# Kernel optimization log

Hardware: AMD Instinct MI355X
Metric: run time of the kernel (lower is better)

Reference implementation:

```python
import jax, jax.numpy as jnp
import numpy as np

N = 50000      # nodes
E = 800000     # edges
IN_DIM = 16
D = 128        # latent_dim == d_model == num_heads*d_head
H = 8
DH = 16
DFF = 512
L = 3          # n_layers
CLAMP = 5.0
EPS = 1e-5


def _layer_norm(x, g, b):
    mu = jnp.mean(x, axis=-1, keepdims=True)
    var = jnp.mean((x - mu) ** 2, axis=-1, keepdims=True)
    return (x - mu) * jax.lax.rsqrt(var + EPS) * g + b


def setup_inputs() -> dict:
    key = jax.random.key(0)
    ks = jax.random.split(key, 16)
    def w(k, shape, fan_in):
        return jax.random.normal(k, shape, dtype=jnp.float32) * (1.0 / np.sqrt(fan_in))
    inp = {
        "nf": jax.random.normal(ks[0], (N, IN_DIM), dtype=jnp.float32),
        "src": jax.random.randint(ks[1], (E,), 0, N, dtype=jnp.int32),
        "dst": jax.random.randint(ks[2], (E,), 0, N, dtype=jnp.int32),
        "enc_W": w(ks[3], (D, IN_DIM), IN_DIM),
        "enc_b": jnp.zeros((D,), jnp.float32),
        "Wq": w(ks[4], (L, H * DH, D), D),
        "Wk": w(ks[5], (L, H * DH, D), D),
        "Wv": w(ks[6], (L, H * DH, D), D),
        "Wo": w(ks[7], (L, D, H * DH), H * DH),
        "ln1_g": jnp.ones((L, D), jnp.float32),
        "ln1_b": jnp.zeros((L, D), jnp.float32),
        "ffn_W1": w(ks[8], (L, DFF, D), D),
        "ffn_b1": jnp.zeros((L, DFF), jnp.float32),
        "ffn_W2": w(ks[9], (L, D, DFF), DFF),
        "ffn_b2": jnp.zeros((L, D), jnp.float32),
        "ln2_g": jnp.ones((L, D), jnp.float32),
        "ln2_b": jnp.zeros((L, D), jnp.float32),
        "dec_W": w(ks[10], (1, D), D),
        "dec_b": jnp.zeros((1,), jnp.float32),
    }
    return inp


def reference(nf, src, dst, enc_W, enc_b, Wq, Wk, Wv, Wo, ln1_g, ln1_b,
              ffn_W1, ffn_b1, ffn_W2, ffn_b2, ln2_g, ln2_b, dec_W, dec_b):
    h = nf @ enc_W.T + enc_b                       # [N, D]
    scale = 1.0 / np.sqrt(DH)
    for l in range(L):
        q = h @ Wq[l].T                            # [N, H*DH]
        k = h @ Wk[l].T
        v = h @ Wv[l].T
        qe = q[dst].reshape(E, H, DH)              # per-edge gather (dst query)
        ke = k[src].reshape(E, H, DH)
        u = jnp.sum(qe * ke, axis=-1) * scale      # [E, H]
        u = jnp.clip(u, -CLAMP, CLAMP)
        # edge_softmax: normalize over edges sharing the same dst node
        m = jax.ops.segment_max(u, dst, num_segments=N)   # [N, H]
        e = jnp.exp(u - m[dst])
        s = jax.ops.segment_sum(e, dst, num_segments=N)   # [N, H]
        a = e / s[dst]                             # [E, H]
        av = a[..., None] * v[src].reshape(E, H, DH)      # [E, H, DH]
        sum_av = jax.ops.segment_sum(av.reshape(E, H * DH), dst, num_segments=N)
        uh = sum_av @ Wo[l].T                      # [N, D]
        h1 = _layer_norm(h + uh, ln1_g[l], ln1_b[l])
        f = jax.nn.relu(h1 @ ffn_W1[l].T + ffn_b1[l]) @ ffn_W2[l].T + ffn_b2[l]
        h = _layer_norm(h1 + f, ln2_g[l], ln2_b[l])
    pred = h @ dec_W.T + dec_b                     # [N, 1]
    # BasicReadout('mean') over the single batched graph -> [1, 1]
    return jnp.mean(pred, axis=0, keepdims=True)
```

## Files before the change

### kernel.cpp

```cpp
#include <hip/hip_runtime.h>
#include <math.h>

static constexpr int D   = 128;
static constexpr int DFF = 512;
static constexpr int LAYERS = 3;
static constexpr float CLAMP_V = 5.0f;
static constexpr float LN_EPS = 1e-5f;

typedef unsigned short u16;
typedef unsigned int   u32;
typedef short bf16x8 __attribute__((ext_vector_type(8)));
typedef float f32x4  __attribute__((ext_vector_type(4)));

__device__ inline float4 ld4(const float* p){ return *reinterpret_cast<const float4*>(p); }
__device__ inline u16 f2bf(float f){ u32 u = __float_as_uint(f); return (u16)((u + 0x7fff + ((u>>16)&1)) >> 16); }
__device__ inline float bl(u32 u){ return __uint_as_float(u << 16); }
__device__ inline float bh(u32 u){ return __uint_as_float(u & 0xffff0000u); }

__device__ inline void gload_lds16(const void* g, void* l) {
  __builtin_amdgcn_global_load_lds(
      (const __attribute__((address_space(1))) void*)g,
      (__attribute__((address_space(3))) void*)l, 16, 0, 0);
}

__global__ __launch_bounds__(256) void count_kernel(const int* __restrict__ dst,
                                                    int* __restrict__ deg, int E)
{
  int e = blockIdx.x*256 + threadIdx.x;
  if (e < E) atomicAdd(&deg[dst[e]], 1);
}

__global__ __launch_bounds__(256) void scan_bsum(const int* __restrict__ deg,
                                                 int* __restrict__ bsum, int N)
{
  const int i0 = blockIdx.x*1024 + threadIdx.x*4;
  int s = 0;
  if (i0 + 3 < N) { int4 v = *(const int4*)&deg[i0]; s = v.x+v.y+v.z+v.w; }
  else { for (int t = 0; t < 4; t++) if (i0+t < N) s += deg[i0+t]; }
  #pragma unroll
  for (int off = 1; off < 64; off <<= 1) s += __shfl_xor(s, off);
  __shared__ int ws_[4];
  if ((threadIdx.x & 63) == 0) ws_[threadIdx.x >> 6] = s;
  __syncthreads();
  if (threadIdx.x == 0) bsum[blockIdx.x] = ws_[0]+ws_[1]+ws_[2]+ws_[3];
}

__global__ __launch_bounds__(64) void scan_bbase(int* __restrict__ bsum, int NB)
{
  const int tid = threadIdx.x;
  int base = 0;
  for (int c = 0; c < NB; c += 64) {
    const int idx = c + tid;
    int v = (idx < NB) ? bsum[idx] : 0;
    const int orig = v;
    #pragma unroll
    for (int off = 1; off < 64; off <<= 1) {
      int t = __shfl_up(v, off);
      if (tid >= off) v += t;
    }
    if (idx < NB) bsum[idx] = base + v - orig;
    base += __shfl(v, 63);
  }
}

__global__ __launch_bounds__(256) void scan_write(const int* __restrict__ deg,
    const int* __restrict__ bbase, int* __restrict__ offs, int* __restrict__ cursor, int N)
{
  const int i0 = blockIdx.x*1024 + threadIdx.x*4;
  int v[4] = {0,0,0,0};
  if (i0 + 3 < N) { int4 t = *(const int4*)&deg[i0]; v[0]=t.x; v[1]=t.y; v[2]=t.z; v[3]=t.w; }
  else { for (int t = 0; t < 4; t++) if (i0+t < N) v[t] = deg[i0+t]; }
  const int s = v[0]+v[1]+v[2]+v[3];
  const int lane = threadIdx.x & 63, w = threadIdx.x >> 6;
  int inc = s;
  #pragma unroll
  for (int off = 1; off < 64; off <<= 1) {
    int t = __shfl_up(inc, off);
    if (lane >= off) inc += t;
  }
  __shared__ int wsum[4];
  if (lane == 63) wsum[w] = inc;
  __syncthreads();
  int wb = 0;
  for (int t = 0; t < 4; t++) if (t < w) wb += wsum[t];
  int run = bbase[blockIdx.x] + wb + inc - s;
  #pragma unroll
  for (int t = 0; t < 4; t++) {
    if (i0 + t < N) { offs[i0+t] = run; cursor[i0+t] = run; run += v[t]; }
  }
  if (i0 <= N-1 && N-1 < i0+4) offs[N] = run;
}

__global__ __launch_bounds__(256) void fill_kernel(const int* __restrict__ dst,
    const int* __restrict__ src, int* __restrict__ cursor, int* __restrict__ csr_src, int E)
{
  int e = blockIdx.x*256 + threadIdx.x;
  if (e < E) {
    int p = atomicAdd(&cursor[dst[e]], 1);
    csr_src[p] = src[e];
  }
}

__global__ __launch_bounds__(256) void convert_weights(
    const float* __restrict__ Wq, const float* __restrict__ Wk, const float* __restrict__ Wv,
    const float* __restrict__ Wo, const float* __restrict__ W1, const float* __restrict__ W2,
    u16* __restrict__ out)
{
  const int SQKV = 3*384*128;
  const int SWO  = 3*128*128;
  const int SW1  = 3*512*128;
  const int SW2  = 3*128*512;
  int i = blockIdx.x*256 + threadIdx.x;
  if (i >= SQKV+SWO+SW1+SW2) return;
  float v;
  if (i < SQKV) {
    int l = i / (384*128), rem = i % (384*128);
    int row = rem / 128, col = rem % 128;
    const float* W = (row < 128) ? Wq : ((row < 256) ? Wk : Wv);
    v = W[(size_t)l*128*128 + (size_t)(row & 127)*128 + col];
  } else if (i < SQKV+SWO) {
    v = Wo[i - SQKV];
  } else if (i < SQKV+SWO+SW1) {
    v = W1[i - SQKV - SWO];
  } else {
    v = W2[i - SQKV - SWO - SW1];
  }
  out[i] = f2bf(v);
}

__global__ __launch_bounds__(256) void encoder_kernel(
    const float* __restrict__ nf, const float* __restrict__ W,
    const float* __restrict__ b, float* __restrict__ h, u16* __restrict__ hb, int N)
{
  int n = blockIdx.x*2 + (threadIdx.x >> 7);
  int d = threadIdx.x & 127;
  if (n >= N) return;
  const float* nr = nf + (size_t)n*16;
  const float* wr = W  + (size_t)d*16;
  float s = b[d];
  #pragma unroll
  for (int kk = 0; kk < 16; kk++) s = fmaf(nr[kk], wr[kk], s);
  h[(size_t)n*D + d]  = s;
  hb[(size_t)n*D + d] = f2bf(s);
}

__device__ inline void mfma_step128(const u16* __restrict__ la, const u16* __restrict__ lb,
                                    int lane, int wr, int wc, f32x4 (&acc)[4][4])
{
  #pragma unroll
  for (int k2 = 0; k2 < 2; k2++) {
    bf16x8 af[4], bfr[4];
    const int kq = k2*4 + (lane >> 4);
    #pragma unroll
    for (int mi = 0; mi < 4; mi++) {
      const int r = wr*64 + mi*16 + (lane & 15);
      af[mi] = *(const bf16x8*)&la[r*64 + ((kq ^ (r & 7)) << 3)];
    }
    #pragma unroll
    for (int ni = 0; ni < 4; ni++) {
      const int r = wc*64 + ni*16 + (lane & 15);
      bfr[ni] = *(const bf16x8*)&lb[r*64 + ((kq ^ (r & 7)) << 3)];
    }
    #pragma unroll
    for (int mi = 0; mi < 4; mi++)
      #pragma unroll
      for (int ni = 0; ni < 4; ni++)
        acc[mi][ni] = __builtin_amdgcn_mfma_f32_16x16x32_bf16(af[mi], bfr[ni], acc[mi][ni], 0, 0, 0);
  }
}

__device__ inline void mfma_stage64(const u16* __restrict__ Atile, const u16* __restrict__ Btile,
                                    int lane, int wr, int wc, int kabase, f32x4 (&acc)[2][4])
{
  #pragma unroll
  for (int k2 = 0; k2 < 2; k2++) {
    const int kql = k2*4 + (lane >> 4);
    const int kqa = kabase + kql;
    bf16x8 af[2], bfr[4];
    #pragma unroll
    for (int mi = 0; mi < 2; mi++) {
      const int r = wr*32 + mi*16 + (lane & 15);
      const int slot = ((kqa & 7) ^ (r & 7)) | (kqa & 8);
      af[mi] = *(const bf16x8*)&Atile[r*128 + slot*8];
    }
    #pragma unroll
    for (int ni = 0; ni < 4; ni++) {
      const int r = wc*64 + ni*16 + (lane & 15);
      bfr[ni] = *(const bf16x8*)&Btile[r*64 + ((kql ^ (r & 7)) << 3)];
    }
    #pragma unroll
    for (int mi = 0; mi < 2; mi++)
      #pragma unroll
      for (int ni = 0; ni < 4; ni++)
        acc[mi][ni] = __builtin_amdgcn_mfma_f32_16x16x32_bf16(af[mi], bfr[ni], acc[mi][ni], 0, 0, 0);
  }
}

__global__ __launch_bounds__(256) void gemm_qkv(
    const u16* __restrict__ A, const u16* __restrict__ B,
    float* __restrict__ qf, u16* __restrict__ kvb, int M)
{
  __shared__ u16 lA[2][128*64];
  __shared__ u16 lB[2][128*64];
  const int sY = blockIdx.y;
  const int m0 = blockIdx.x * 128;
  const int tid = threadIdx.x, lane = tid & 63, wid = tid >> 6;
  const int wr = wid >> 1, wc = wid & 1;
  const int ldrow = lane >> 3;
  const int gran  = (lane & 7) ^ ldrow;
  const u16* Bm = B + (size_t)sY*128*128;

  f32x4 acc[4][4];
  #pragma unroll
  for (int i = 0; i < 4; i++)
    #pragma unroll
    for (int j = 0; j < 4; j++) { acc[i][j][0]=0.f; acc[i][j][1]=0.f; acc[i][j][2]=0.f; acc[i][j][3]=0.f; }

  auto issue = [&](int ks) {
    const int k0 = ks*64 + gran*8;
    #pragma unroll
    for (int is = 0; is < 4; is++) {
      const int r = wid*32 + is*8;
      int gm = m0 + r + ldrow; if (gm >= M) gm = M - 1;
      gload_lds16(A + (size_t)gm*128 + k0, &lA[ks][r*64]);
      gload_lds16(Bm + (size_t)(r + ldrow)*128 + k0, &lB[ks][r*64]);
    }
  };

  issue(0);
  asm volatile("s_waitcnt vmcnt(0)" ::: "memory");
  __syncthreads();
  issue(1);
  mfma_step128(lA[0], lB[0], lane, wr, wc, acc);
  asm volatile("s_waitcnt vmcnt(0)" ::: "memory");
  __syncthreads();
  mfma_step128(lA[1], lB[1], lane, wr, wc, acc);

  const int rbase = m0 + wr*64 + ((lane >> 4) << 2);
  const int cbase = wc*64 + (lane & 15);
  #pragma unroll
  for (int ni = 0; ni < 4; ni++) {
    const int col = cbase + ni*16;
    #pragma unroll
    for (int mi = 0; mi < 4; mi++) {
      #pragma unroll
      for (int r = 0; r < 4; r++) {
        const int gm = rbase + mi*16 + r;
        if (gm < M) {
          if (sY == 0) qf[(size_t)gm*128 + col] = acc[mi][ni][r];
          else         kvb[(size_t)gm*256 + (sY-1)*128 + col] = f2bf(acc[mi][ni][r]);
        }
      }
    }
  }
}

__global__ __launch_bounds__(256) void ffn_fused(
    const u16* __restrict__ savb, const u16* __restrict__ Wo,
    const u16* __restrict__ W1,   const u16* __restrict__ W2,
    const float* __restrict__ ln1g, const float* __restrict__ ln1b,
    const float* __restrict__ b1,   const float* __restrict__ b2,
    const float* __restrict__ ln2g, const float* __restrict__ ln2b,
    float* __restrict__ hf, u16* __restrict__ hb, int M)
{
  __shared__ u16 lB[2][128*64];
  __shared__ u16 h1s[64*128];
  __shared__ u16 fs[64*128];
  __shared__ float lsum[64][2];
  __shared__ float lsq[64][2];

  const int tid  = threadIdx.x;
  const int lane = tid & 63;
  const int wid  = tid >> 6;
  const int wr   = wid >> 1, wc = wid & 1;
  const int m0   = blockIdx.x * 64;

  const int ldrow = lane >> 3;
  const int gran  = (lane & 7) ^ ldrow;

  const int rbase_l = wr*32 + ((lane >> 4) << 2);
  const int cbase   = wc*64 + (lane & 15);

  auto stage_issue = [&](int s) {
    u16* dst = lB[s & 1];
    #pragma unroll
    for (int is = 0; is < 4; is++) {
      const int r = wid*32 + is*8;
      const u16* gp;
      if (s < 2) gp = Wo + (size_t)(r + ldrow)*128 + s*64;
      else {
        const int t = s - 2, c = t >> 2, k = t & 3;
        gp = (k < 2) ? (W1 + (size_t)(c*128 + r + ldrow)*128 + k*64)
                     : (W2 + (size_t)(r + ldrow)*512 + c*128 + (k-2)*64);
      }
      gload_lds16(gp + gran*8, dst + r*64);
    }
  };

  #pragma unroll
  for (int is = 0; is < 4; is++) {
    const int r0 = wid*16 + is*4;
    const int rr = r0 + (lane >> 4);
    int gm = m0 + rr; if (gm >= M) gm = M - 1;
    const int gsrc = ((lane & 7) ^ (rr & 7)) | (lane & 8);
    gload_lds16(savb + (size_t)gm*128 + gsrc*8, &fs[r0*128]);
  }
  stage_issue(0);

  f32x4 acc1[2][4], acc2[2][4], acc3[2][4];
  #pragma unroll
  for (int i = 0; i < 2; i++)
    #pragma unroll
    for (int j = 0; j < 4; j++) {
      acc1[i][j][0]=0.f; acc1[i][j][1]=0.f; acc1[i][j][2]=0.f; acc1[i][j][3]=0.f;
      acc3[i][j][0]=0.f; acc3[i][j][1]=0.f; acc3[i][j][2]=0.f; acc3[i][j][3]=0.f;
    }

  asm volatile("s_waitcnt vmcnt(0)" ::: "memory");
  __syncthreads();

  #pragma unroll
  for (int s = 0; s < 18; s++) {
    if (s < 17) stage_issue(s + 1);

    if (s >= 2 && ((s - 2) & 3) == 0) {
      #pragma unroll
      for (int i = 0; i < 2; i++)
        #pragma unroll
        for (int j = 0; j < 4; j++) { acc2[i][j][0]=0.f; acc2[i][j][1]=0.f; acc2[i][j][2]=0.f; acc2[i][j][3]=0.f; }
    }

    if (s < 2)
      mfma_stage64(fs,  lB[s & 1], lane, wr, wc, (s & 1)*8, acc1);
    else if (((s - 2) & 3) < 2)
      mfma_stage64(h1s, lB[s & 1], lane, wr, wc, (s & 1)*8, acc2);
    else
      mfma_stage64(fs,  lB[s & 1], lane, wr, wc, (s & 1)*8, acc3);

    if (s == 1) {
      #pragma unroll
      for (int mi = 0; mi < 2; mi++) {
        #pragma unroll
        for (int r = 0; r < 4; r++) {
          const int lrow = rbase_l + mi*16 + r;
          int gr = m0 + lrow; if (gr >= M) gr = M - 1;
          float ps = 0.f, pq = 0.f;
          #pragma unroll
          for (int ni = 0; ni < 4; ni++) {
            const int col = cbase + ni*16;
            float x = acc1[mi][ni][r] + hf[(size_t)gr*128 + col];
            acc1[mi][ni][r] = x;
            ps += x; pq += x*x;
          }
          #pragma unroll
          for (int off = 1; off < 16; off <<= 1) { ps += __shfl_xor(ps, off); pq += __shfl_xor(pq, off); }
          if ((lane & 15) == 0) { lsum[lrow][wc] = ps; lsq[lrow][wc] = pq; }
        }
      }
      __syncthreads();
      #pragma unroll
      for (int mi = 0; mi < 2; mi++) {
        #pragma unroll
        for (int r = 0; r < 4; r++) {
          const int lrow = rbase_l + mi*16 + r;
          const float mean = (lsum[lrow][0] + lsum[lrow][1]) * (1.0f/128.0f);
          float var = (lsq[lrow][0] + lsq[lrow][1]) * (1.0f/128.0f) - mean*mean;
          const float rstd = rsqrtf(fmaxf(var, 0.f) + LN_EPS);
          #pragma unroll
          for (int ni = 0; ni < 4; ni++) {
            const int col = cbase + ni*16;
            float o = (acc1[mi][ni][r] - mean) * rstd * ln1g[col] + ln1b[col];
            acc1[mi][ni][r] = o;
            const int g16 = col >> 3;
            const int slot = ((g16 & 7) ^ (lrow & 7)) | (g16 & 8);
            h1s[lrow*128 + slot*8 + (col & 7)] = f2bf(o);
          }
        }
      }
    } else if (s >= 2 && ((s - 2) & 3) == 1) {
      const int c = (s - 2) >> 2;
      #pragma unroll
      for (int mi = 0; mi < 2; mi++) {
        #pragma unroll
        for (int r = 0; r < 4; r++) {
          const int lrow = rbase_l + mi*16 + r;
          #pragma unroll
          for (int ni = 0; ni < 4; ni++) {
            const int col = cbase + ni*16;
            float v = fmaxf(acc2[mi][ni][r] + b1[c*128 + col], 0.f);
            const int g16 = col >> 3;
            const int slot = ((g16 & 7) ^ (lrow & 7)) | (g16 & 8);
            fs[lrow*128 + slot*8 + (col & 7)] = f2bf(v);
          }
        }
      }
    }

    if (s < 17) {
      asm volatile("s_waitcnt vmcnt(0)" ::: "memory");
      __syncthreads();
    }
  }

  #pragma unroll
  for (int mi = 0; mi < 2; mi++) {
    #pragma unroll
    for (int r = 0; r < 4; r++) {
      const int lrow = rbase_l + mi*16 + r;
      float ps = 0.f, pq = 0.f;
      #pragma unroll
      for (int ni = 0; ni < 4; ni++) {
        const int col = cbase + ni*16;
        float x = acc3[mi][ni][r] + b2[col] + acc1[mi][ni][r];
        acc3[mi][ni][r] = x;
        ps += x; pq += x*x;
      }
      #pragma unroll
      for (int off = 1; off < 16; off <<= 1) { ps += __shfl_xor(ps, off); pq += __shfl_xor(pq, off); }
      if ((lane & 15) == 0) { lsum[lrow][wc] = ps; lsq[lrow][wc] = pq; }
    }
  }
  __syncthreads();
  #pragma unroll
  for (int mi = 0; mi < 2; mi++) {
    #pragma unroll
    for (int r = 0; r < 4; r++) {
      const int lrow = rbase_l + mi*16 + r;
      const int grow = m0 + lrow;
      if (grow >= M) continue;
      const float mean = (lsum[lrow][0] + lsum[lrow][1]) * (1.0f/128.0f);
      float var = (lsq[lrow][0] + lsq[lrow][1]) * (1.0f/128.0f) - mean*mean;
      const float rstd = rsqrtf(fmaxf(var, 0.f) + LN_EPS);
      #pragma unroll
      for (int ni = 0; ni < 4; ni++) {
        const int col = cbase + ni*16;
        float o = (acc3[mi][ni][r] - mean) * rstd * ln2g[col] + ln2b[col];
        hf[(size_t)grow*128 + col] = o;
        hb[(size_t)grow*128 + col] = f2bf(o);
      }
    }
  }
}

__global__ __launch_bounds__(256) void attn_kernel(
    const float* __restrict__ q, const u16* __restrict__ kv,
    const int* __restrict__ offs, const int* __restrict__ csr_src,
    u16* __restrict__ outb, int N)
{
  const int tid = threadIdx.x;
  const int j   = tid & 15;
  const int n   = blockIdx.x*16 + (tid >> 4);
  if (n >= N) return;

  float qreg[8];
  *(float4*)&qreg[0] = ld4(&q[(size_t)n*128 + j*8]);
  *(float4*)&qreg[4] = ld4(&q[(size_t)n*128 + j*8 + 4]);

  const int start = offs[n];
  const int deg   = offs[n+1] - start;

  float s = 0.f;
  float acc[8] = {0,0,0,0,0,0,0,0};
  const int gb = tid & 48;

  for (int base = 0; base < deg; base += 16) {
    const int myidx = base + j;
    const int sn_mine = (myidx < deg) ? csr_src[start + myidx] : 0;
    const int cnt = (deg - base < 16) ? (deg - base) : 16;

    for (int b2 = 0; b2 < cnt; b2 += 8) {
      const int m8 = cnt - b2;
      uint4 K4[8], V4[8];
      #pragma unroll
      for (int u = 0; u < 8; u++) {
        const int sel = b2 + ((u < m8) ? u : 0);
        const int sn = __shfl(sn_mine, gb + sel);
        const u16* row = kv + (size_t)sn*256 + j*8;
        K4[u] = *(const uint4*)row;
        V4[u] = *(const uint4*)(row + 128);
      }
      #pragma unroll
      for (int u = 0; u < 8; u++) {
        if (u < m8) {
          float d = bl(K4[u].x)*qreg[0] + bh(K4[u].x)*qreg[1]
                  + bl(K4[u].y)*qreg[2] + bh(K4[u].y)*qreg[3]
                  + bl(K4[u].z)*qreg[4] + bh(K4[u].z)*qreg[5]
                  + bl(K4[u].w)*qreg[6] + bh(K4[u].w)*qreg[7];
          d += __shfl_xor(d, 1);
          float uu = fminf(fmaxf(d * 0.25f, -CLAMP_V), CLAMP_V);
          float e = __expf(uu - CLAMP_V);
          s += e;
          acc[0] = fmaf(e, bl(V4[u].x), acc[0]);
          acc[1] = fmaf(e, bh(V4[u].x), acc[1]);
          acc[2] = fmaf(e, bl(V4[u].y), acc[2]);
          acc[3] = fmaf(e, bh(V4[u].y), acc[3]);
          acc[4] = fmaf(e, bl(V4[u].z), acc[4]);
          acc[5] = fmaf(e, bh(V4[u].z), acc[5]);
          acc[6] = fmaf(e, bl(V4[u].w), acc[6]);
          acc[7] = fmaf(e, bh(V4[u].w), acc[7]);
        }
      }
    }
  }

  const float rs = (deg > 0) ? (1.0f / s) : 0.f;
  u16 o[8];
  #pragma unroll
  for (int t = 0; t < 8; t++) o[t] = f2bf(acc[t] * rs);
  *(uint4*)&outb[(size_t)n*128 + j*8] = *(const uint4*)o;
}

__global__ __launch_bounds__(256) void dec_partial(const float* __restrict__ h,
    const float* __restrict__ W, float* __restrict__ partials, int N)
{
  float acc = 0.f;
  for (int n = blockIdx.x*256 + threadIdx.x; n < N; n += 256*256) {
    const float* hr = h + (size_t)n*D;
    float s = 0.f;
    #pragma unroll
    for (int t = 0; t < 32; t++) {
      float4 hv = ld4(&hr[t*4]); float4 wv = ld4(&W[t*4]);
      s += hv.x*wv.x + hv.y*wv.y + hv.z*wv.z + hv.w*wv.w;
    }
    acc += s;
  }
  #pragma unroll
  for (int off = 1; off < 64; off <<= 1) acc += __shfl_xor(acc, off);
  __shared__ float red[4];
  int lane = threadIdx.x & 63, w = threadIdx.x >> 6;
  if (lane == 0) red[w] = acc;
  __syncthreads();
  if (threadIdx.x == 0) partials[blockIdx.x] = red[0]+red[1]+red[2]+red[3];
}

__global__ __launch_bounds__(256) void dec_final(const float* __restrict__ partials,
    const float* __restrict__ decb, float* __restrict__ out, int N)
{
  float a = partials[threadIdx.x];
  #pragma unroll
  for (int off = 1; off < 64; off <<= 1) a += __shfl_xor(a, off);
  __shared__ float red[4];
  int lane = threadIdx.x & 63, w = threadIdx.x >> 6;
  if (lane == 0) red[w] = a;
  __syncthreads();
  if (threadIdx.x == 0) out[0] = (red[0]+red[1]+red[2]+red[3]) / (float)N + decb[0];
}

extern "C" void kernel_launch(void* const* d_in, const int* in_sizes, int n_in,
                              void* d_out, int out_size, void* d_ws, size_t ws_size,
                              hipStream_t stream)
{
  const float* nf   = (const float*)d_in[0];
  const int*   src  = (const int*)  d_in[1];
  const int*   dst  = (const int*)  d_in[2];
  const float* encW = (const float*)d_in[3];
  const float* encb = (const float*)d_in[4];
  const float* Wq   = (const float*)d_in[5];
  const float* Wk   = (const float*)d_in[6];
  const float* Wv   = (const float*)d_in[7];
  const float* Wo   = (const float*)d_in[8];
  const float* ln1g = (const float*)d_in[9];
  const float* ln1b = (const float*)d_in[10];
  const float* W1   = (const float*)d_in[11];
  const float* b1   = (const float*)d_in[12];
  const float* W2   = (const float*)d_in[13];
  const float* b2   = (const float*)d_in[14];
  const float* ln2g = (const float*)d_in[15];
  const float* ln2b = (const float*)d_in[16];
  const float* decW = (const float*)d_in[17];
  const float* decb = (const float*)d_in[18];
  float* out = (float*)d_out;

  const int N = in_sizes[0] / 16;
  const int E = in_sizes[1];
  const int NB = (N + 1023) / 1024;

  float* ws   = (float*)d_ws;
  float* h    = ws;
  float* q    = h  + (size_t)N*128;
  u16*  hb    = (u16*)(q + (size_t)N*128);
  u16*  kvb   = hb  + (size_t)N*128;
  u16*  savb  = kvb + (size_t)N*256;
  int* deg    = (int*)(savb + (size_t)N*128);
  int* offs   = deg + N;
  int* cursor = offs + N + 1;
  int* csr    = cursor + N;
  int* bsum   = csr + E;
  float* partials = (float*)(bsum + ((NB + 255) & ~255));
  u16* wbuf   = (u16*)(partials + 512);
  u16* wqkv   = wbuf;
  u16* wo_b   = wbuf + 147456;
  u16* w1_b   = wbuf + 196608;
  u16* w2_b   = wbuf + 393216;

  hipMemsetAsync(deg, 0, sizeof(int)*N, stream);
  count_kernel<<<(E+255)/256, 256, 0, stream>>>(dst, deg, E);
  scan_bsum<<<NB, 256, 0, stream>>>(deg, bsum, N);
  scan_bbase<<<1, 64, 0, stream>>>(bsum, NB);
  scan_write<<<NB, 256, 0, stream>>>(deg, bsum, offs, cursor, N);
  fill_kernel<<<(E+255)/256, 256, 0, stream>>>(dst, src, cursor, csr, E);

  convert_weights<<<(589824+255)/256, 256, 0, stream>>>(Wq, Wk, Wv, Wo, W1, W2, wbuf);

  encoder_kernel<<<(N+1)/2, 256, 0, stream>>>(nf, encW, encb, h, hb, N);

  const int gmx = (N + 127)/128;
  for (int l = 0; l < LAYERS; l++) {
    const u16* wqkv_l = wqkv + (size_t)l*384*128;
    const u16* wo_l   = wo_b + (size_t)l*128*128;
    const u16* w1_l   = w1_b + (size_t)l*512*128;
    const u16* w2_l   = w2_b + (size_t)l*128*512;

    gemm_qkv<<<dim3(gmx,3), 256, 0, stream>>>(hb, wqkv_l, q, kvb, N);

    attn_kernel<<<(N+15)/16, 256, 0, stream>>>(q, kvb, offs, csr, savb, N);

    ffn_fused<<<(N+63)/64, 256, 0, stream>>>(
        savb, wo_l, w1_l, w2_l,
        ln1g + l*D, ln1b + l*D, b1 + l*DFF, b2 + l*D, ln2g + l*D, ln2b + l*D,
        h, hb, N);
  }

  dec_partial<<<256, 256, 0, stream>>>(h, decW, partials, N);
  dec_final<<<1, 256, 0, stream>>>(partials, decb, out, N);
}
```

Before: 556.4 us.

## Reuse A tile across Q/K/V in one block; widen attention gather batch

The QKV GEMM now loads each 128-row activation tile into LDS once and loops over the three weight matrices with double-buffered weight tiles, instead of launching a 3-wide grid that reloads A per matrix. This removes redundant activation reads but cuts the grid to a third, lowering parallelism (about 391 blocks). Separately, the attention kernel issues all 16 neighbor K/V gathers at once instead of two batches of 8, raising memory-level parallelism at the cost of more registers.

```diff
diff --git a/kernel.cpp b/kernel.cpp
--- a/kernel.cpp
+++ b/kernel.cpp
@@ -201,56 +201,72 @@
     float* __restrict__ qf, u16* __restrict__ kvb, int M)
 {
   __shared__ u16 lA[2][128*64];
-  __shared__ u16 lB[2][128*64];
-  const int sY = blockIdx.y;
+  __shared__ u16 lW[2][128*64];
   const int m0 = blockIdx.x * 128;
   const int tid = threadIdx.x, lane = tid & 63, wid = tid >> 6;
   const int wr = wid >> 1, wc = wid & 1;
   const int ldrow = lane >> 3;
   const int gran  = (lane & 7) ^ ldrow;
-  const u16* Bm = B + (size_t)sY*128*128;
-
-  f32x4 acc[4][4];
-  #pragma unroll
-  for (int i = 0; i < 4; i++)
-    #pragma unroll
-    for (int j = 0; j < 4; j++) { acc[i][j][0]=0.f; acc[i][j][1]=0.f; acc[i][j][2]=0.f; acc[i][j][3]=0.f; }
-
-  auto issue = [&](int ks) {
+
+  auto issueA = [&](int ks) {
     const int k0 = ks*64 + gran*8;
     #pragma unroll
     for (int is = 0; is < 4; is++) {
       const int r = wid*32 + is*8;
       int gm = m0 + r + ldrow; if (gm >= M) gm = M - 1;
       gload_lds16(A + (size_t)gm*128 + k0, &lA[ks][r*64]);
-      gload_lds16(Bm + (size_t)(r + ldrow)*128 + k0, &lB[ks][r*64]);
     }
   };
-
-  issue(0);
+  auto issueW = [&](int s) {
+    const u16* Bm = B + (size_t)(s >> 1)*128*128;
+    const int k0 = (s & 1)*64 + gran*8;
+    #pragma unroll
+    for (int is = 0; is < 4; is++) {
+      const int r = wid*32 + is*8;
+      gload_lds16(Bm + (size_t)(r + ldrow)*128 + k0, &lW[s & 1][r*64]);
+    }
+  };
+
+  issueA(0); issueA(1); issueW(0);
+
+  f32x4 acc[4][4];
+  const int rbase = m0 + wr*64 + ((lane >> 4) << 2);
+  const int cbase = wc*64 + (lane & 15);
+
   asm volatile("s_waitcnt vmcnt(0)" ::: "memory");
   __syncthreads();
-  issue(1);
-  mfma_step128(lA[0], lB[0], lane, wr, wc, acc);
-  asm volatile("s_waitcnt vmcnt(0)" ::: "memory");
-  __syncthreads();
-  mfma_step128(lA[1], lB[1], lane, wr, wc, acc);
-
-  const int rbase = m0 + wr*64 + ((lane >> 4) << 2);
-  const int cbase = wc*64 + (lane & 15);
-  #pragma unroll
-  for (int ni = 0; ni < 4; ni++) {
-    const int col = cbase + ni*16;
-    #pragma unroll
-    for (int mi = 0; mi < 4; mi++) {
-      #pragma unroll
-      for (int r = 0; r < 4; r++) {
-        const int gm = rbase + mi*16 + r;
-        if (gm < M) {
-          if (sY == 0) qf[(size_t)gm*128 + col] = acc[mi][ni][r];
-          else         kvb[(size_t)gm*256 + (sY-1)*128 + col] = f2bf(acc[mi][ni][r]);
+
+  #pragma unroll
+  for (int s = 0; s < 6; s++) {
+    if (s < 5) issueW(s + 1);
+    if ((s & 1) == 0) {
+      #pragma unroll
+      for (int i = 0; i < 4; i++)
+        #pragma unroll
+        for (int j = 0; j < 4; j++) { acc[i][j][0]=0.f; acc[i][j][1]=0.f; acc[i][j][2]=0.f; acc[i][j][3]=0.f; }
+    }
+    mfma_step128(lA[s & 1], lW[s & 1], lane, wr, wc, acc);
+    if (s & 1) {
+      const int mat = s >> 1;
+      #pragma unroll
+      for (int ni = 0; ni < 4; ni++) {
+        const int col = cbase + ni*16;
+        #pragma unroll
+        for (int mi = 0; mi < 4; mi++) {
+          #pragma unroll
+          for (int r = 0; r < 4; r++) {
+            const int gm = rbase + mi*16 + r;
+            if (gm < M) {
+              if (mat == 0) qf[(size_t)gm*128 + col] = acc[mi][ni][r];
+              else          kvb[(size_t)gm*256 + (mat-1)*128 + col] = f2bf(acc[mi][ni][r]);
+            }
+          }
         }
       }
+    }
+    if (s < 5) {
+      asm volatile("s_waitcnt vmcnt(0)" ::: "memory");
+      __syncthreads();
     }
   }
 }
@@ -468,37 +484,34 @@
     const int sn_mine = (myidx < deg) ? csr_src[start + myidx] : 0;
     const int cnt = (deg - base < 16) ? (deg - base) : 16;
 
-    for (int b2 = 0; b2 < cnt; b2 += 8) {
-      const int m8 = cnt - b2;
-      uint4 K4[8], V4[8];
-      #pragma unroll
-      for (int u = 0; u < 8; u++) {
-        const int sel = b2 + ((u < m8) ? u : 0);
-        const int sn = __shfl(sn_mine, gb + sel);
-        const u16* row = kv + (size_t)sn*256 + j*8;
-        K4[u] = *(const uint4*)row;
-        V4[u] = *(const uint4*)(row + 128);
-      }
-      #pragma unroll
-      for (int u = 0; u < 8; u++) {
-        if (u < m8) {
-          float d = bl(K4[u].x)*qreg[0] + bh(K4[u].x)*qreg[1]
-                  + bl(K4[u].y)*qreg[2] + bh(K4[u].y)*qreg[3]
-                  + bl(K4[u].z)*qreg[4] + bh(K4[u].z)*qreg[5]
-                  + bl(K4[u].w)*qreg[6] + bh(K4[u].w)*qreg[7];
-          d += __shfl_xor(d, 1);
-          float uu = fminf(fmaxf(d * 0.25f, -CLAMP_V), CLAMP_V);
-          float e = __expf(uu - CLAMP_V);
-          s += e;
-          acc[0] = fmaf(e, bl(V4[u].x), acc[0]);
-          acc[1] = fmaf(e, bh(V4[u].x), acc[1]);
-          acc[2] = fmaf(e, bl(V4[u].y), acc[2]);
-          acc[3] = fmaf(e, bh(V4[u].y), acc[3]);
-          acc[4] = fmaf(e, bl(V4[u].z), acc[4]);
-          acc[5] = fmaf(e, bh(V4[u].z), acc[5]);
-          acc[6] = fmaf(e, bl(V4[u].w), acc[6]);
-          acc[7] = fmaf(e, bh(V4[u].w), acc[7]);
-        }
+    uint4 K4[16], V4[16];
+    #pragma unroll
+    for (int u = 0; u < 16; u++) {
+      const int sel = (u < cnt) ? u : 0;
+      const int sn = __shfl(sn_mine, gb + sel);
+      const u16* row = kv + (size_t)sn*256 + j*8;
+      K4[u] = *(const uint4*)row;
+      V4[u] = *(const uint4*)(row + 128);
+    }
+    #pragma unroll
+    for (int u = 0; u < 16; u++) {
+      if (u < cnt) {
+        float d = bl(K4[u].x)*qreg[0] + bh(K4[u].x)*qreg[1]
+                + bl(K4[u].y)*qreg[2] + bh(K4[u].y)*qreg[3]
+                + bl(K4[u].z)*qreg[4] + bh(K4[u].z)*qreg[5]
+                + bl(K4[u].w)*qreg[6] + bh(K4[u].w)*qreg[7];
+        d += __shfl_xor(d, 1);
+        float uu = fminf(fmaxf(d * 0.25f, -CLAMP_V), CLAMP_V);
+        float e = __expf(uu - CLAMP_V);
+        s += e;
+        acc[0] = fmaf(e, bl(V4[u].x), acc[0]);
+        acc[1] = fmaf(e, bh(V4[u].x), acc[1]);
+        acc[2] = fmaf(e, bl(V4[u].y), acc[2]);
+        acc[3] = fmaf(e, bh(V4[u].y), acc[3]);
+        acc[4] = fmaf(e, bl(V4[u].z), acc[4]);
+        acc[5] = fmaf(e, bh(V4[u].z), acc[5]);
+        acc[6] = fmaf(e, bl(V4[u].w), acc[6]);
+        acc[7] = fmaf(e, bh(V4[u].w), acc[7]);
       }
     }
   }
@@ -611,7 +624,7 @@
     const u16* w1_l   = w1_b + (size_t)l*512*128;
     const u16* w2_l   = w2_b + (size_t)l*128*512;
 
-    gemm_qkv<<<dim3(gmx,3), 256, 0, stream>>>(hb, wqkv_l, q, kvb, N);
+    gemm_qkv<<<gmx, 256, 0, stream>>>(hb, wqkv_l, q, kvb, N);
 
     attn_kernel<<<(N+15)/16, 256, 0, stream>>>(q, kvb, offs, csr, savb, N);
 
```

Measured after the change: 541.9 us. -2.6%, faster.

## Fuse QKV projection into encoder and into previous layer's FFN epilogue

Applied to the files above, without the earlier changes.

Fuses the encoder with the first layer's QKV GEMM, and appends the next layer's Q/K/V projections to the FFN kernel. The new LayerNorm output is kept in LDS as bf16 and reused as the A operand, so the separate gemm_qkv launches and the bf16 h buffer round-trip go away. In exchange the FFN kernel runs six more pipeline stages per block, with more registers and longer blocks. The QKV GEMM now uses 64-row tiles instead of 128-row tiles.

```diff
diff --git a/kernel.cpp b/kernel.cpp
--- a/kernel.cpp
+++ b/kernel.cpp
@@ -128,47 +128,6 @@
   out[i] = f2bf(v);
 }
 
-__global__ __launch_bounds__(256) void encoder_kernel(
-    const float* __restrict__ nf, const float* __restrict__ W,
-    const float* __restrict__ b, float* __restrict__ h, u16* __restrict__ hb, int N)
-{
-  int n = blockIdx.x*2 + (threadIdx.x >> 7);
-  int d = threadIdx.x & 127;
-  if (n >= N) return;
-  const float* nr = nf + (size_t)n*16;
-  const float* wr = W  + (size_t)d*16;
-  float s = b[d];
-  #pragma unroll
-  for (int kk = 0; kk < 16; kk++) s = fmaf(nr[kk], wr[kk], s);
-  h[(size_t)n*D + d]  = s;
-  hb[(size_t)n*D + d] = f2bf(s);
-}
-
-__device__ inline void mfma_step128(const u16* __restrict__ la, const u16* __restrict__ lb,
-                                    int lane, int wr, int wc, f32x4 (&acc)[4][4])
-{
-  #pragma unroll
-  for (int k2 = 0; k2 < 2; k2++) {
-    bf16x8 af[4], bfr[4];
-    const int kq = k2*4 + (lane >> 4);
-    #pragma unroll
-    for (int mi = 0; mi < 4; mi++) {
-      const int r = wr*64 + mi*16 + (lane & 15);
-      af[mi] = *(const bf16x8*)&la[r*64 + ((kq ^ (r & 7)) << 3)];
-    }
-    #pragma unroll
-    for (int ni = 0; ni < 4; ni++) {
-      const int r = wc*64 + ni*16 + (lane & 15);
-      bfr[ni] = *(const bf16x8*)&lb[r*64 + ((kq ^ (r & 7)) << 3)];
-    }
-    #pragma unroll
-    for (int mi = 0; mi < 4; mi++)
-      #pragma unroll
-      for (int ni = 0; ni < 4; ni++)
-        acc[mi][ni] = __builtin_amdgcn_mfma_f32_16x16x32_bf16(af[mi], bfr[ni], acc[mi][ni], 0, 0, 0);
-  }
-}
-
 __device__ inline void mfma_stage64(const u16* __restrict__ Atile, const u16* __restrict__ Btile,
                                     int lane, int wr, int wc, int kabase, f32x4 (&acc)[2][4])
 {
@@ -196,72 +155,122 @@
   }
 }
 
-__global__ __launch_bounds__(256) void gemm_qkv(
-    const u16* __restrict__ A, const u16* __restrict__ B,
-    float* __restrict__ qf, u16* __restrict__ kvb, int M)
-{
-  __shared__ u16 lA[2][128*64];
+__global__ __launch_bounds__(256) void enc_qkv(
+    const float* __restrict__ nf, const float* __restrict__ encW, const float* __restrict__ encb,
+    const u16* __restrict__ Wqkv,
+    float* __restrict__ hf, float* __restrict__ qf, u16* __restrict__ kvb, int M)
+{
   __shared__ u16 lB[2][128*64];
-  const int sY = blockIdx.y;
-  const int m0 = blockIdx.x * 128;
-  const int tid = threadIdx.x, lane = tid & 63, wid = tid >> 6;
-  const int wr = wid >> 1, wc = wid & 1;
+  __shared__ u16 h1s[64*128];
+
+  const int tid  = threadIdx.x;
+  const int lane = tid & 63;
+  const int wid  = tid >> 6;
+  const int wr   = wid >> 1, wc = wid & 1;
+  const int m0   = blockIdx.x * 64;
   const int ldrow = lane >> 3;
   const int gran  = (lane & 7) ^ ldrow;
-  const u16* Bm = B + (size_t)sY*128*128;
-
-  f32x4 acc[4][4];
-  #pragma unroll
-  for (int i = 0; i < 4; i++)
-    #pragma unroll
-    for (int j = 0; j < 4; j++) { acc[i][j][0]=0.f; acc[i][j][1]=0.f; acc[i][j][2]=0.f; acc[i][j][3]=0.f; }
-
-  auto issue = [&](int ks) {
-    const int k0 = ks*64 + gran*8;
+  const int rbase_l = wr*32 + ((lane >> 4) << 2);
+  const int cbase   = wc*64 + (lane & 15);
+
+  auto stage_issue = [&](int s) {
+    u16* dst = lB[s & 1];
+    const u16* Bm = Wqkv + (size_t)(s >> 1)*128*128;
+    const int k0 = (s & 1)*64 + gran*8;
     #pragma unroll
     for (int is = 0; is < 4; is++) {
       const int r = wid*32 + is*8;
-      int gm = m0 + r + ldrow; if (gm >= M) gm = M - 1;
-      gload_lds16(A + (size_t)gm*128 + k0, &lA[ks][r*64]);
-      gload_lds16(Bm + (size_t)(r + ldrow)*128 + k0, &lB[ks][r*64]);
+      gload_lds16(Bm + (size_t)(r + ldrow)*128 + k0, dst + r*64);
     }
   };
-
-  issue(0);
+  stage_issue(0);
+
+  f32x4 hacc[2][4];
+  #pragma unroll
+  for (int mi = 0; mi < 2; mi++) {
+    #pragma unroll
+    for (int r = 0; r < 4; r++) {
+      const int lrow = rbase_l + mi*16 + r;
+      int grow = m0 + lrow; if (grow >= M) grow = M - 1;
+      const float* nr = nf + (size_t)grow*16;
+      float nfr[16];
+      #pragma unroll
+      for (int t = 0; t < 4; t++) *(float4*)&nfr[t*4] = ld4(&nr[t*4]);
+      #pragma unroll
+      for (int ni = 0; ni < 4; ni++) {
+        const int col = cbase + ni*16;
+        const float* wrow = encW + (size_t)col*16;
+        float s = encb[col];
+        #pragma unroll
+        for (int kk = 0; kk < 16; kk++) s = fmaf(nfr[kk], wrow[kk], s);
+        hacc[mi][ni][r] = s;
+      }
+    }
+  }
+  #pragma unroll
+  for (int mi = 0; mi < 2; mi++) {
+    #pragma unroll
+    for (int r = 0; r < 4; r++) {
+      const int lrow = rbase_l + mi*16 + r;
+      const int grow = m0 + lrow;
+      #pragma unroll
+      for (int ni = 0; ni < 4; ni++) {
+        const int col = cbase + ni*16;
+        const float o = hacc[mi][ni][r];
+        if (grow < M) hf[(size_t)grow*128 + col] = o;
+        const int g16 = col >> 3;
+        const int slot = ((g16 & 7) ^ (lrow & 7)) | (g16 & 8);
+        h1s[lrow*128 + slot*8 + (col & 7)] = f2bf(o);
+      }
+    }
+  }
   asm volatile("s_waitcnt vmcnt(0)" ::: "memory");
   __syncthreads();
-  issue(1);
-  mfma_step128(lA[0], lB[0], lane, wr, wc, acc);
-  asm volatile("s_waitcnt vmcnt(0)" ::: "memory");
-  __syncthreads();
-  mfma_step128(lA[1], lB[1], lane, wr, wc, acc);
-
-  const int rbase = m0 + wr*64 + ((lane >> 4) << 2);
-  const int cbase = wc*64 + (lane & 15);
-  #pragma unroll
-  for (int ni = 0; ni < 4; ni++) {
-    const int col = cbase + ni*16;
-    #pragma unroll
-    for (int mi = 0; mi < 4; mi++) {
-      #pragma unroll
-      for (int r = 0; r < 4; r++) {
-        const int gm = rbase + mi*16 + r;
-        if (gm < M) {
-          if (sY == 0) qf[(size_t)gm*128 + col] = acc[mi][ni][r];
-          else         kvb[(size_t)gm*256 + (sY-1)*128 + col] = f2bf(acc[mi][ni][r]);
-        }
-      }
-    }
-  }
-}
-
+
+  f32x4 acc[2][4];
+  #pragma unroll
+  for (int s = 0; s < 6; s++) {
+    if (s < 5) stage_issue(s + 1);
+    if ((s & 1) == 0) {
+      #pragma unroll
+      for (int i = 0; i < 2; i++)
+        #pragma unroll
+        for (int j = 0; j < 4; j++) { acc[i][j][0]=0.f; acc[i][j][1]=0.f; acc[i][j][2]=0.f; acc[i][j][3]=0.f; }
+    }
+    mfma_stage64(h1s, lB[s & 1], lane, wr, wc, (s & 1)*8, acc);
+    if (s & 1) {
+      const int mat = s >> 1;
+      #pragma unroll
+      for (int mi = 0; mi < 2; mi++) {
+        #pragma unroll
+        for (int r = 0; r < 4; r++) {
+          const int grow = m0 + rbase_l + mi*16 + r;
+          if (grow >= M) continue;
+          #pragma unroll
+          for (int ni = 0; ni < 4; ni++) {
+            const int col = cbase + ni*16;
+            if (mat == 0) qf[(size_t)grow*128 + col] = acc[mi][ni][r];
+            else          kvb[(size_t)grow*256 + (mat-1)*128 + col] = f2bf(acc[mi][ni][r]);
+          }
+        }
+      }
+    }
+    if (s < 5) {
+      asm volatile("s_waitcnt vmcnt(0)" ::: "memory");
+      __syncthreads();
+    }
+  }
+}
+
+template<bool QKV>
 __global__ __launch_bounds__(256) void ffn_fused(
     const u16* __restrict__ savb, const u16* __restrict__ Wo,
     const u16* __restrict__ W1,   const u16* __restrict__ W2,
+    const u16* __restrict__ Wqkv,
     const float* __restrict__ ln1g, const float* __restrict__ ln1b,
     const float* __restrict__ b1,   const float* __restrict__ b2,
     const float* __restrict__ ln2g, const float* __restrict__ ln2b,
-    float* __restrict__ hf, u16* __restrict__ hb, int M)
+    float* __restrict__ hf, float* __restrict__ qf, u16* __restrict__ kvb, int M)
 {
   __shared__ u16 lB[2][128*64];
   __shared__ u16 h1s[64*128];
@@ -281,6 +290,8 @@
   const int rbase_l = wr*32 + ((lane >> 4) << 2);
   const int cbase   = wc*64 + (lane & 15);
 
+  constexpr int NS = QKV ? 24 : 18;
+
   auto stage_issue = [&](int s) {
     u16* dst = lB[s & 1];
     #pragma unroll
@@ -288,10 +299,13 @@
       const int r = wid*32 + is*8;
       const u16* gp;
       if (s < 2) gp = Wo + (size_t)(r + ldrow)*128 + s*64;
-      else {
+      else if (s < 18) {
         const int t = s - 2, c = t >> 2, k = t & 3;
         gp = (k < 2) ? (W1 + (size_t)(c*128 + r + ldrow)*128 + k*64)
                      : (W2 + (size_t)(r + ldrow)*512 + c*128 + (k-2)*64);
+      } else {
+        const int t = s - 18, mat = t >> 1, k = t & 1;
+        gp = Wqkv + (size_t)mat*128*128 + (size_t)(r + ldrow)*128 + k*64;
       }
       gload_lds16(gp + gran*8, dst + r*64);
     }
@@ -320,10 +334,10 @@
   __syncthreads();
 
   #pragma unroll
-  for (int s = 0; s < 18; s++) {
-    if (s < 17) stage_issue(s + 1);
-
-    if (s >= 2 && ((s - 2) & 3) == 0) {
+  for (int s = 0; s < NS; s++) {
+    if (s < NS-1) stage_issue(s + 1);
+
+    if ((s >= 2 && s < 18 && ((s - 2) & 3) == 0) || (s >= 18 && ((s - 18) & 1) == 0)) {
       #pragma unroll
       for (int i = 0; i < 2; i++)
         #pragma unroll
@@ -332,10 +346,13 @@
 
     if (s < 2)
       mfma_stage64(fs,  lB[s & 1], lane, wr, wc, (s & 1)*8, acc1);
-    else if (((s - 2) & 3) < 2)
+    else if (s < 18) {
+      if (((s - 2) & 3) < 2)
+        mfma_stage64(h1s, lB[s & 1], lane, wr, wc, (s & 1)*8, acc2);
+      else
+        mfma_stage64(fs,  lB[s & 1], lane, wr, wc, (s & 1)*8, acc3);
+    } else
       mfma_stage64(h1s, lB[s & 1], lane, wr, wc, (s & 1)*8, acc2);
-    else
-      mfma_stage64(fs,  lB[s & 1], lane, wr, wc, (s & 1)*8, acc3);
 
     if (s == 1) {
       #pragma unroll
@@ -377,7 +394,7 @@
           }
         }
       }
-    } else if (s >= 2 && ((s - 2) & 3) == 1) {
+    } else if (s >= 2 && s < 18 && ((s - 2) & 3) == 1) {
       const int c = (s - 2) >> 2;
       #pragma unroll
       for (int mi = 0; mi < 2; mi++) {
@@ -394,50 +411,69 @@
           }
         }
       }
-    }
-
-    if (s < 17) {
+    } else if (s == 17) {
+      #pragma unroll
+      for (int mi = 0; mi < 2; mi++) {
+        #pragma unroll
+        for (int r = 0; r < 4; r++) {
+          const int lrow = rbase_l + mi*16 + r;
+          float ps = 0.f, pq = 0.f;
+          #pragma unroll
+          for (int ni = 0; ni < 4; ni++) {
+            const int col = cbase + ni*16;
+            float x = acc3[mi][ni][r] + b2[col] + acc1[mi][ni][r];
+            acc3[mi][ni][r] = x;
+            ps += x; pq += x*x;
+          }
+          #pragma unroll
+          for (int off = 1; off < 16; off <<= 1) { ps += __shfl_xor(ps, off); pq += __shfl_xor(pq, off); }
+          if ((lane & 15) == 0) { lsum[lrow][wc] = ps; lsq[lrow][wc] = pq; }
+        }
+      }
+      __syncthreads();
+      #pragma unroll
+      for (int mi = 0; mi < 2; mi++) {
+        #pragma unroll
+        for (int r = 0; r < 4; r++) {
+          const int lrow = rbase_l + mi*16 + r;
+          const int grow = m0 + lrow;
+          const float mean = (lsum[lrow][0] + lsum[lrow][1]) * (1.0f/128.0f);
+          float var = (lsq[lrow][0] + lsq[lrow][1]) * (1.0f/128.0f) - mean*mean;
+          const float rstd = rsqrtf(fmaxf(var, 0.f) + LN_EPS);
+          #pragma unroll
+          for (int ni = 0; ni < 4; ni++) {
+            const int col = cbase + ni*16;
+            float o = (acc3[mi][ni][r] - mean) * rstd * ln2g[col] + ln2b[col];
+            if (grow < M) hf[(size_t)grow*128 + col] = o;
+            if (QKV) {
+              const int g16 = col >> 3;
+              const int slot = ((g16 & 7) ^ (lrow & 7)) | (g16 & 8);
+              h1s[lrow*128 + slot*8 + (col & 7)] = f2bf(o);
+            }
+          }
+        }
+      }
+    } else if (QKV && s >= 19 && (s & 1)) {
+      const int mat = (s - 19) >> 1;
+      #pragma unroll
+      for (int mi = 0; mi < 2; mi++) {
+        #pragma unroll
+        for (int r = 0; r < 4; r++) {
+          const int grow = m0 + rbase_l + mi*16 + r;
+          if (grow >= M) continue;
+          #pragma unroll
+          for (int ni = 0; ni < 4; ni++) {
+            const int col = cbase + ni*16;
+            if (mat == 0) qf[(size_t)grow*128 + col] = acc2[mi][ni][r];
+            else          kvb[(size_t)grow*256 + (mat-1)*128 + col] = f2bf(acc2[mi][ni][r]);
+          }
+        }
+      }
+    }
+
+    if (s < NS-1) {
       asm volatile("s_waitcnt vmcnt(0)" ::: "memory");
       __syncthreads();
-    }
-  }
-
-  #pragma unroll
-  for (int mi = 0; mi < 2; mi++) {
-    #pragma unroll
-    for (int r = 0; r < 4; r++) {
-      const int lrow = rbase_l + mi*16 + r;
-      float ps = 0.f, pq = 0.f;
-      #pragma unroll
-      for (int ni = 0; ni < 4; ni++) {
-        const int col = cbase + ni*16;
-        float x = acc3[mi][ni][r] + b2[col] + acc1[mi][ni][r];
-        acc3[mi][ni][r] = x;
-        ps += x; pq += x*x;
-      }
-      #pragma unroll
-      for (int off = 1; off < 16; off <<= 1) { ps += __shfl_xor(ps, off); pq += __shfl_xor(pq, off); }
-      if ((lane & 15) == 0) { lsum[lrow][wc] = ps; lsq[lrow][wc] = pq; }
-    }
-  }
-  __syncthreads();
-  #pragma unroll
-  for (int mi = 0; mi < 2; mi++) {
-    #pragma unroll
-    for (int r = 0; r < 4; r++) {
-      const int lrow = rbase_l + mi*16 + r;
-      const int grow = m0 + lrow;
-      if (grow >= M) continue;
-      const float mean = (lsum[lrow][0] + lsum[lrow][1]) * (1.0f/128.0f);
-      float var = (lsq[lrow][0] + lsq[lrow][1]) * (1.0f/128.0f) - mean*mean;
-      const float rstd = rsqrtf(fmaxf(var, 0.f) + LN_EPS);
-      #pragma unroll
-      for (int ni = 0; ni < 4; ni++) {
-        const int col = cbase + ni*16;
-        float o = (acc3[mi][ni][r] - mean) * rstd * ln2g[col] + ln2b[col];
-        hf[(size_t)grow*128 + col] = o;
-        hb[(size_t)grow*128 + col] = f2bf(o);
-      }
     }
   }
 }
@@ -578,8 +614,7 @@
   float* ws   = (float*)d_ws;
   float* h    = ws;
   float* q    = h  + (size_t)N*128;
-  u16*  hb    = (u16*)(q + (size_t)N*128);
-  u16*  kvb   = hb  + (size_t)N*128;
+  u16*  kvb   = (u16*)(q + (size_t)N*128);
   u16*  savb  = kvb + (size_t)N*256;
   int* deg    = (int*)(savb + (size_t)N*128);
   int* offs   = deg + N;
@@ -602,23 +637,28 @@
 
   convert_weights<<<(589824+255)/256, 256, 0, stream>>>(Wq, Wk, Wv, Wo, W1, W2, wbuf);
 
-  encoder_kernel<<<(N+1)/2, 256, 0, stream>>>(nf, encW, encb, h, hb, N);
-
-  const int gmx = (N + 127)/128;
+  const int g64 = (N + 63)/64;
+
+  enc_qkv<<<g64, 256, 0, stream>>>(nf, encW, encb, wqkv, h, q, kvb, N);
+
   for (int l = 0; l < LAYERS; l++) {
-    const u16* wqkv_l = wqkv + (size_t)l*384*128;
     const u16* wo_l   = wo_b + (size_t)l*128*128;
     const u16* w1_l   = w1_b + (size_t)l*512*128;
     const u16* w2_l   = w2_b + (size_t)l*128*512;
-
-    gemm_qkv<<<dim3(gmx,3), 256, 0, stream>>>(hb, wqkv_l, q, kvb, N);
+    const u16* wqkv_n = wqkv + (size_t)(l+1)*384*128;
 
     attn_kernel<<<(N+15)/16, 256, 0, stream>>>(q, kvb, offs, csr, savb, N);
 
-    ffn_fused<<<(N+63)/64, 256, 0, stream>>>(
-        savb, wo_l, w1_l, w2_l,
-        ln1g + l*D, ln1b + l*D, b1 + l*DFF, b2 + l*D, ln2g + l*D, ln2b + l*D,
-        h, hb, N);
+    if (l < LAYERS-1)
+      ffn_fused<true><<<g64, 256, 0, stream>>>(
+          savb, wo_l, w1_l, w2_l, wqkv_n,
+          ln1g + l*D, ln1b + l*D, b1 + l*DFF, b2 + l*D, ln2g + l*D, ln2b + l*D,
+          h, q, kvb, N);
+    else
+      ffn_fused<false><<<g64, 256, 0, stream>>>(
+          savb, wo_l, w1_l, w2_l, nullptr,
+          ln1g + l*D, ln1b + l*D, b1 + l*DFF, b2 + l*D, ln2g + l*D, ln2b + l*D,
+          h, nullptr, nullptr, N);
   }
 
   dec_partial<<<256, 256, 0, stream>>>(h, decW, partials, N);
```

Result: slower. 765.4 us (+37.6%).
